# Kernel tuning notes

Hardware: AMD Instinct MI355X
Metric: run time of the kernel (lower is better)

The kernel has to match this reference:

```python
import jax, jax.numpy as jnp
import numpy as np

HEADS = 4
EPS = 1e-5

def _layernorm(x, g, b):
    mu = jnp.mean(x, axis=-1, keepdims=True)
    var = jnp.var(x, axis=-1, keepdims=True)
    return (x - mu) / jnp.sqrt(var + EPS) * g + b

def setup_inputs() -> dict:
    key = jax.random.key(0)
    ks = jax.random.split(key, 16)
    N, dim, k, G = 400000, 256, 1, 4096
    h = jax.random.normal(ks[0], (N, dim), dtype=jnp.float32)
    batch = jnp.sort(jax.random.randint(ks[1], (N,), 0, G).astype(jnp.int64))
    s = 1.0 / np.sqrt(dim)
    return {
        "h": h,
        "batch": batch,
        "num_graphs": G,
        "seed": jax.random.normal(ks[2], (k, dim), dtype=jnp.float32),
        "in_proj_w": jax.random.uniform(ks[3], (3 * dim, dim), minval=-s, maxval=s, dtype=jnp.float32),
        "in_proj_b": jnp.zeros((3 * dim,), jnp.float32),
        "out_w": jax.random.uniform(ks[4], (dim, dim), minval=-s, maxval=s, dtype=jnp.float32),
        "out_b": jnp.zeros((dim,), jnp.float32),
        "w1": jax.random.uniform(ks[5], (4 * dim, dim), minval=-s, maxval=s, dtype=jnp.float32),
        "b1": jnp.zeros((4 * dim,), jnp.float32),
        "w2": jax.random.uniform(ks[6], (dim, 4 * dim), minval=-1.0 / np.sqrt(4 * dim), maxval=1.0 / np.sqrt(4 * dim), dtype=jnp.float32),
        "b2": jnp.zeros((dim,), jnp.float32),
        "g1": jnp.ones((dim,), jnp.float32),
        "beta1": jnp.zeros((dim,), jnp.float32),
        "g2": jnp.ones((dim,), jnp.float32),
        "beta2": jnp.zeros((dim,), jnp.float32),
    }

def reference(h, batch, num_graphs, seed, in_proj_w, in_proj_b, out_w, out_b,
              w1, b1, w2, b2, g1, beta1, g2, beta2):
    N, dim = h.shape
    k = seed.shape[0]
    hd = dim // HEADS
    G = num_graphs
    # q/k/v projections (torch MHA packed in_proj: rows [0:dim]=Q, [dim:2dim]=K, [2dim:]=V)
    q = seed @ in_proj_w[:dim].T + in_proj_b[:dim]                 # [k, dim]
    kk = h @ in_proj_w[dim:2 * dim].T + in_proj_b[dim:2 * dim]     # [N, dim]
    vv = h @ in_proj_w[2 * dim:].T + in_proj_b[2 * dim:]           # [N, dim]
    qh = q.reshape(k, HEADS, hd).transpose(1, 0, 2)                # [H, k, hd]
    kh = kk.reshape(N, HEADS, hd)                                  # [N, H, hd]
    vh = vv.reshape(N, HEADS, hd)                                  # [N, H, hd]
    scale = 1.0 / np.sqrt(hd)
    scores = jnp.einsum('hkd,nhd->nhk', qh, kh) * scale            # [N, H, k]
    # segment softmax over nodes of each graph
    smax = jax.ops.segment_max(scores, batch, num_segments=G)      # [G, H, k]
    e = jnp.exp(scores - smax[batch])                              # [N, H, k]
    denom = jax.ops.segment_sum(e, batch, num_segments=G)          # [G, H, k]
    wv = jax.ops.segment_sum(e[:, :, :, None] * vh[:, :, None, :], batch, num_segments=G)  # [G, H, k, hd]
    attn = jnp.where(denom[..., None] > 0, wv / jnp.maximum(denom, 1e-9)[..., None], 0.0)
    attn = attn.transpose(0, 2, 1, 3).reshape(G, k, dim)           # [G, k, dim]
    o = attn @ out_w.T + out_b                                     # [G, k, dim]
    x = _layernorm(o + seed[None, :, :], g1, beta1)
    f = jax.nn.relu(x @ w1.T + b1) @ w2.T + b2
    x = _layernorm(x + f, g2, beta2)
    # empty graphs output zeros (matches torch loop)
    count = jax.ops.segment_sum(jnp.ones((N,), jnp.float32), batch, num_segments=G)
    return jnp.where((count > 0)[:, None, None], x, 0.0)
```

## Files before the change

### kernel.cpp

```cpp
#include <hip/hip_runtime.h>
#include <hip/hip_bf16.h>


#define DIM 256
#define CHUNK 32

typedef short bf16x8 __attribute__((ext_vector_type(8)));
typedef float f32x4  __attribute__((ext_vector_type(4)));
#define MFMA16(a, b, c) __builtin_amdgcn_mfma_f32_16x16x32_bf16(a, b, c, 0, 0, 0)

#define OFF_C      0
#define OFF_D      1024
#define OFF_CONST  1040
#define OFF_P2B    2048
#define OFF_W1B    133120
#define OFF_W2B    264192
#define OFF_TB     395264
#define OFF_X1     2492416
#define OFF_X1B    3540992
#define OFF_UB     4065280
#define OFF_CNT    6162432

__global__ __launch_bounds__(256) void prep_all_kernel(
    const float* __restrict__ seed, const float* __restrict__ ipw,
    const float* __restrict__ ipb, const float* __restrict__ out_w,
    const float* __restrict__ out_b, const float* __restrict__ w1,
    const float* __restrict__ w2,
    float* __restrict__ cvec, float* __restrict__ dconst,
    float* __restrict__ constvec, __hip_bfloat16* __restrict__ P2b,
    __hip_bfloat16* __restrict__ w1b, __hip_bfloat16* __restrict__ w2b)
{
    int b = blockIdx.x, t = threadIdx.x;
    __shared__ float q_s[DIM];
    if (b < 1024) {
        int i = b >> 2, hD = b & 3;
        float a = 0.f;
        for (int j = 0; j < 64; ++j)
            a += out_w[i * DIM + hD * 64 + j]
               * ipw[(size_t)(2 * DIM + hD * 64 + j) * DIM + t];
        P2b[(size_t)i * 1024 + hD * DIM + t] = __float2bfloat16(a);
    } else if (b == 1024) {
        const float scale = 0.125f;
        float acc = ipb[t];
        for (int d = 0; d < DIM; ++d) acc += seed[d] * ipw[t * DIM + d];
        q_s[t] = acc;
        __syncthreads();
        for (int hh = 0; hh < 4; ++hh) {
            float a = 0.f;
            for (int j = 0; j < 64; ++j)
                a += q_s[hh * 64 + j] * ipw[(size_t)(DIM + hh * 64 + j) * DIM + t];
            cvec[hh * DIM + t] = a * scale;
        }
        if (t < 4) {
            float a = 0.f;
            for (int j = 0; j < 64; ++j)
                a += q_s[t * 64 + j] * ipb[DIM + t * 64 + j];
            dconst[t] = a * scale;
        }
        float cc = out_b[t];
        for (int c = 0; c < DIM; ++c)
            cc += out_w[t * DIM + c] * ipb[2 * DIM + c];
        constvec[t] = cc;
    } else if (b < 1153) {
        int base = (b - 1025) * 2048 + t;
        for (int i = 0; i < 8; ++i)
            w1b[base + i * 256] = __float2bfloat16(w1[base + i * 256]);
    } else {
        int base = (b - 1153) * 2048 + t;
        for (int i = 0; i < 8; ++i)
            w2b[base + i * 256] = __float2bfloat16(w2[base + i * 256]);
    }
}

__global__ __launch_bounds__(256) void attn_pool_kernel(
    const float* __restrict__ hmat, const int* __restrict__ batch,
    const float* __restrict__ cvec, const float* __restrict__ dconst,
    __hip_bfloat16* __restrict__ Tb, int* __restrict__ cnt, int N)
{
    int g = blockIdx.x;
    int tid = threadIdx.x;
    int lane = tid & 63, wave = tid >> 6;

    __shared__ float hbuf[CHUNK][DIM];
    __shared__ float4 esc[CHUNK];
    __shared__ float lred[4][4];

    int s, e;
    { int l = 0, r = N;
      while (l < r) { int m = (l + r) >> 1; if (batch[m] < g) l = m + 1; else r = m; }
      s = l; }
    { int l = s, r = N;
      while (l < r) { int m = (l + r) >> 1; if (batch[m] < g + 1) l = m + 1; else r = m; }
      e = l; }

    if (tid == 0) cnt[g] = e - s;
    size_t tbase = (size_t)g * 1024;
    if (e == s) {
        __hip_bfloat16 z = __float2bfloat16(0.f);
        Tb[tbase + tid] = z; Tb[tbase + 256 + tid] = z;
        Tb[tbase + 512 + tid] = z; Tb[tbase + 768 + tid] = z;
        return;
    }

    int hh = lane & 3, seg = lane >> 2;
    const float* cb = cvec + hh * DIM + seg * 16;
    float4 cr0 = *(const float4*)(cb + 0);
    float4 cr1 = *(const float4*)(cb + 4);
    float4 cr2 = *(const float4*)(cb + 8);
    float4 cr3 = *(const float4*)(cb + 12);
    float dc_mine = dconst[hh];

    float S0 = 0.f, S1 = 0.f, S2 = 0.f, S3 = 0.f;
    float lp = 0.f;

    for (int n0 = s; n0 < e; n0 += CHUNK) {
        int ccnt = min(CHUNK, e - n0);
        for (int idx = tid; idx < ccnt * 64; idx += 256) {
            int j = idx >> 6, q4 = idx & 63;
            float4 v = *(const float4*)&hmat[(size_t)(n0 + j) * DIM + q4 * 4];
            *(float4*)&hbuf[j][q4 * 4] = v;
        }
        __syncthreads();

        for (int j = wave; j < ccnt; j += 4) {
            const float* hb = &hbuf[j][seg * 16];
            float4 h0 = *(const float4*)(hb + 0);
            float4 h1 = *(const float4*)(hb + 4);
            float4 h2 = *(const float4*)(hb + 8);
            float4 h3 = *(const float4*)(hb + 12);
            float p = h0.x * cr0.x + h0.y * cr0.y + h0.z * cr0.z + h0.w * cr0.w
                    + h1.x * cr1.x + h1.y * cr1.y + h1.z * cr1.z + h1.w * cr1.w
                    + h2.x * cr2.x + h2.y * cr2.y + h2.z * cr2.z + h2.w * cr2.w
                    + h3.x * cr3.x + h3.y * cr3.y + h3.z * cr3.z + h3.w * cr3.w;
            p += __shfl_xor(p, 4);
            p += __shfl_xor(p, 8);
            p += __shfl_xor(p, 16);
            p += __shfl_xor(p, 32);
            if (lane < 4) {
                float ev = __expf(p + dc_mine);
                ((float*)&esc[j])[lane] = ev;
                lp += ev;
            }
        }
        __syncthreads();

        for (int j = 0; j < ccnt; ++j) {
            float4 e4 = esc[j];
            float hv = hbuf[j][tid];
            S0 = fmaf(e4.x, hv, S0); S1 = fmaf(e4.y, hv, S1);
            S2 = fmaf(e4.z, hv, S2); S3 = fmaf(e4.w, hv, S3);
        }
        __syncthreads();
    }

    if (lane < 4) lred[wave][lane] = lp;
    __syncthreads();
    float l0 = lred[0][0] + lred[1][0] + lred[2][0] + lred[3][0];
    float l1 = lred[0][1] + lred[1][1] + lred[2][1] + lred[3][1];
    float l2 = lred[0][2] + lred[1][2] + lred[2][2] + lred[3][2];
    float l3 = lred[0][3] + lred[1][3] + lred[2][3] + lred[3][3];
    Tb[tbase + tid]       = __float2bfloat16(S0 / l0);
    Tb[tbase + 256 + tid] = __float2bfloat16(S1 / l1);
    Tb[tbase + 512 + tid] = __float2bfloat16(S2 / l2);
    Tb[tbase + 768 + tid] = __float2bfloat16(S3 / l3);
}

__global__ __launch_bounds__(64) void gemm_o_ln1_kernel(
    const __hip_bfloat16* __restrict__ Tb, const __hip_bfloat16* __restrict__ P2b,
    const float* __restrict__ constvec, const float* __restrict__ seed,
    const float* __restrict__ g1, const float* __restrict__ be1,
    float* __restrict__ x1, __hip_bfloat16* __restrict__ x1b)
{
    int m0 = blockIdx.x * 16;
    int lane = threadIdx.x, quad = lane >> 4, l16 = lane & 15;
    f32x4 acc[16];
#pragma unroll
    for (int i = 0; i < 16; ++i) acc[i] = (f32x4){0.f, 0.f, 0.f, 0.f};
    const __hip_bfloat16* Ap = Tb + (size_t)(m0 + l16) * 1024 + quad * 8;
    const __hip_bfloat16* Bp = P2b + (size_t)l16 * 1024 + quad * 8;
    for (int k0 = 0; k0 < 1024; k0 += 32) {
        bf16x8 a = *(const bf16x8*)(Ap + k0);
#pragma unroll
        for (int nt = 0; nt < 16; ++nt) {
            bf16x8 b = *(const bf16x8*)(Bp + (size_t)nt * 16 * 1024 + k0);
            acc[nt] = MFMA16(a, b, acc[nt]);
        }
    }
    float v[16][4];
    float sum[4] = {0, 0, 0, 0}, sq[4] = {0, 0, 0, 0};
#pragma unroll
    for (int nt = 0; nt < 16; ++nt) {
        int col = nt * 16 + l16;
        float cv = constvec[col] + seed[col];
#pragma unroll
        for (int r = 0; r < 4; ++r) {
            float x = acc[nt][r] + cv;
            v[nt][r] = x; sum[r] += x; sq[r] += x * x;
        }
    }
    float mu_r[4], rs_r[4];
#pragma unroll
    for (int r = 0; r < 4; ++r) {
        float s_ = sum[r], q_ = sq[r];
        s_ += __shfl_xor(s_, 1);  q_ += __shfl_xor(q_, 1);
        s_ += __shfl_xor(s_, 2);  q_ += __shfl_xor(q_, 2);
        s_ += __shfl_xor(s_, 4);  q_ += __shfl_xor(q_, 4);
        s_ += __shfl_xor(s_, 8);  q_ += __shfl_xor(q_, 8);
        float mu = s_ * (1.f / 256);
        float var = q_ * (1.f / 256) - mu * mu;
        mu_r[r] = mu;
        rs_r[r] = rsqrtf(fmaxf(var, 0.f) + 1e-5f);
    }
#pragma unroll
    for (int nt = 0; nt < 16; ++nt) {
        int col = nt * 16 + l16;
        float gg = g1[col], bb = be1[col];
#pragma unroll
        for (int r = 0; r < 4; ++r) {
            int gr = m0 + quad * 4 + r;
            float y = (v[nt][r] - mu_r[r]) * rs_r[r] * gg + bb;
            x1[(size_t)gr * 256 + col] = y;
            x1b[(size_t)gr * 256 + col] = __float2bfloat16(y);
        }
    }
}

__global__ __launch_bounds__(64) void gemm_u_kernel(
    const __hip_bfloat16* __restrict__ x1b, const __hip_bfloat16* __restrict__ w1b,
    const float* __restrict__ b1, __hip_bfloat16* __restrict__ ub)
{
    int m0 = blockIdx.x * 16, nb0 = blockIdx.y * 128;
    int lane = threadIdx.x, quad = lane >> 4, l16 = lane & 15;
    f32x4 acc[8];
#pragma unroll
    for (int i = 0; i < 8; ++i) acc[i] = (f32x4){0.f, 0.f, 0.f, 0.f};
    const __hip_bfloat16* Ap = x1b + (size_t)(m0 + l16) * 256 + quad * 8;
    const __hip_bfloat16* Bp = w1b + (size_t)(nb0 + l16) * 256 + quad * 8;
#pragma unroll
    for (int k0 = 0; k0 < 256; k0 += 32) {
        bf16x8 a = *(const bf16x8*)(Ap + k0);
#pragma unroll
        for (int nt = 0; nt < 8; ++nt) {
            bf16x8 b = *(const bf16x8*)(Bp + (size_t)nt * 16 * 256 + k0);
            acc[nt] = MFMA16(a, b, acc[nt]);
        }
    }
#pragma unroll
    for (int nt = 0; nt < 8; ++nt) {
        int col = nb0 + nt * 16 + l16;
        float bb = b1[col];
#pragma unroll
        for (int r = 0; r < 4; ++r) {
            int gr = m0 + quad * 4 + r;
            float y = fmaxf(acc[nt][r] + bb, 0.f);
            ub[(size_t)gr * 1024 + col] = __float2bfloat16(y);
        }
    }
}

__global__ __launch_bounds__(64) void gemm_f_ln2_kernel(
    const __hip_bfloat16* __restrict__ ub, const __hip_bfloat16* __restrict__ w2b,
    const float* __restrict__ b2, const float* __restrict__ x1,
    const float* __restrict__ g2, const float* __restrict__ be2,
    const int* __restrict__ cnt, float* __restrict__ outp)
{
    int m0 = blockIdx.x * 16;
    int lane = threadIdx.x, quad = lane >> 4, l16 = lane & 15;
    f32x4 acc[16];
#pragma unroll
    for (int i = 0; i < 16; ++i) acc[i] = (f32x4){0.f, 0.f, 0.f, 0.f};
    const __hip_bfloat16* Ap = ub + (size_t)(m0 + l16) * 1024 + quad * 8;
    const __hip_bfloat16* Bp = w2b + (size_t)l16 * 1024 + quad * 8;
    for (int k0 = 0; k0 < 1024; k0 += 32) {
        bf16x8 a = *(const bf16x8*)(Ap + k0);
#pragma unroll
        for (int nt = 0; nt < 16; ++nt) {
            bf16x8 b = *(const bf16x8*)(Bp + (size_t)nt * 16 * 1024 + k0);
            acc[nt] = MFMA16(a, b, acc[nt]);
        }
    }
    float v[16][4];
    float sum[4] = {0, 0, 0, 0}, sq[4] = {0, 0, 0, 0};
#pragma unroll
    for (int nt = 0; nt < 16; ++nt) {
        int col = nt * 16 + l16;
        float bb = b2[col];
#pragma unroll
        for (int r = 0; r < 4; ++r) {
            int gr = m0 + quad * 4 + r;
            float x = acc[nt][r] + bb + x1[(size_t)gr * 256 + col];
            v[nt][r] = x; sum[r] += x; sq[r] += x * x;
        }
    }
    float mu_r[4], rs_r[4];
#pragma unroll
    for (int r = 0; r < 4; ++r) {
        float s_ = sum[r], q_ = sq[r];
        s_ += __shfl_xor(s_, 1);  q_ += __shfl_xor(q_, 1);
        s_ += __shfl_xor(s_, 2);  q_ += __shfl_xor(q_, 2);
        s_ += __shfl_xor(s_, 4);  q_ += __shfl_xor(q_, 4);
        s_ += __shfl_xor(s_, 8);  q_ += __shfl_xor(q_, 8);
        float mu = s_ * (1.f / 256);
        float var = q_ * (1.f / 256) - mu * mu;
        mu_r[r] = mu;
        rs_r[r] = rsqrtf(fmaxf(var, 0.f) + 1e-5f);
    }
#pragma unroll
    for (int r = 0; r < 4; ++r) {
        int gr = m0 + quad * 4 + r;
        float mask = (cnt[gr] > 0) ? 1.f : 0.f;
#pragma unroll
        for (int nt = 0; nt < 16; ++nt) {
            int col = nt * 16 + l16;
            float y = ((v[nt][r] - mu_r[r]) * rs_r[r] * g2[col] + be2[col]) * mask;
            outp[(size_t)gr * 256 + col] = y;
        }
    }
}

extern "C" void kernel_launch(void* const* d_in, const int* in_sizes, int n_in,
                              void* d_out, int out_size, void* d_ws, size_t ws_size,
                              hipStream_t stream) {
    const float* h     = (const float*)d_in[0];
    const int*   batch = (const int*)d_in[1];
    const float* seed  = (const float*)d_in[3];
    const float* ipw   = (const float*)d_in[4];
    const float* ipb   = (const float*)d_in[5];
    const float* out_w = (const float*)d_in[6];
    const float* out_b = (const float*)d_in[7];
    const float* w1    = (const float*)d_in[8];
    const float* b1    = (const float*)d_in[9];
    const float* w2    = (const float*)d_in[10];
    const float* b2    = (const float*)d_in[11];
    const float* g1    = (const float*)d_in[12];
    const float* be1   = (const float*)d_in[13];
    const float* g2    = (const float*)d_in[14];
    const float* be2   = (const float*)d_in[15];

    int N = in_sizes[1];
    int G = out_size / DIM;

    float* ws = (float*)d_ws;
    float* cvec     = ws + OFF_C;
    float* dconst   = ws + OFF_D;
    float* constvec = ws + OFF_CONST;
    __hip_bfloat16* P2b = (__hip_bfloat16*)(ws + OFF_P2B);
    __hip_bfloat16* w1b = (__hip_bfloat16*)(ws + OFF_W1B);
    __hip_bfloat16* w2b = (__hip_bfloat16*)(ws + OFF_W2B);
    __hip_bfloat16* Tb  = (__hip_bfloat16*)(ws + OFF_TB);
    float* x1       = ws + OFF_X1;
    __hip_bfloat16* x1b = (__hip_bfloat16*)(ws + OFF_X1B);
    __hip_bfloat16* ub  = (__hip_bfloat16*)(ws + OFF_UB);
    int*   cnt      = (int*)(ws + OFF_CNT);

    prep_all_kernel<<<1281, 256, 0, stream>>>(seed, ipw, ipb, out_w, out_b, w1, w2,
                                              cvec, dconst, constvec, P2b, w1b, w2b);
    attn_pool_kernel<<<G, 256, 0, stream>>>(h, batch, cvec, dconst, Tb, cnt, N);
    gemm_o_ln1_kernel<<<G / 16, 64, 0, stream>>>(Tb, P2b, constvec, seed, g1, be1,
                                                 x1, x1b);
    gemm_u_kernel<<<dim3(G / 16, 8), 64, 0, stream>>>(x1b, w1b, b1, ub);
    gemm_f_ln2_kernel<<<G / 16, 64, 0, stream>>>(ub, w2b, b2, x1, g2, be2, cnt,
                                                 (float*)d_out);
}
```

Measured before the change: 716.2 us.

## Rewrite attention pooling as single-wave streaming and fuse the three epilogue GEMMs

Segment starts are now computed once in the prep kernel, which removes the per-block binary searches. Attention pooling now runs one 64-thread wave per graph. It streams rows from global memory with register prefetch and keeps all four heads' accumulators in registers, with no LDS staging or block barriers. The out-proj+LN1, FFN up and FFN down+LN2 GEMMs are fused into one kernel, with intermediates held in shared memory, so the global round-trips for x1 and the hidden activations go away. The risks are lower per-graph parallelism in pooling, high register pressure, and the fused epilogue running only G/16 single-wave blocks.

```diff
diff --git a/kernel.cpp b/kernel.cpp
--- a/kernel.cpp
+++ b/kernel.cpp
@@ -3,7 +3,6 @@
 
 
 #define DIM 256
-#define CHUNK 32
 
 typedef short bf16x8 __attribute__((ext_vector_type(8)));
 typedef float f32x4  __attribute__((ext_vector_type(4)));
@@ -16,19 +15,55 @@
 #define OFF_W1B    133120
 #define OFF_W2B    264192
 #define OFF_TB     395264
-#define OFF_X1     2492416
-#define OFF_X1B    3540992
-#define OFF_UB     4065280
-#define OFF_CNT    6162432
+#define OFF_SEG    2492416
+
+__device__ inline float dot16(const float4& a0, const float4& a1,
+                              const float4& a2, const float4& a3,
+                              const float4& b0, const float4& b1,
+                              const float4& b2, const float4& b3) {
+    return a0.x*b0.x + a0.y*b0.y + a0.z*b0.z + a0.w*b0.w
+         + a1.x*b1.x + a1.y*b1.y + a1.z*b1.z + a1.w*b1.w
+         + a2.x*b2.x + a2.y*b2.y + a2.z*b2.z + a2.w*b2.w
+         + a3.x*b3.x + a3.y*b3.y + a3.z*b3.z + a3.w*b3.w;
+}
+
+__device__ inline void fma4(float e, const float4& v, float4& s) {
+    s.x = fmaf(e, v.x, s.x); s.y = fmaf(e, v.y, s.y);
+    s.z = fmaf(e, v.z, s.z); s.w = fmaf(e, v.w, s.w);
+}
+
+__device__ inline float4 xred(float4 a) {
+    a.x += __shfl_xor(a.x, 16); a.y += __shfl_xor(a.y, 16);
+    a.z += __shfl_xor(a.z, 16); a.w += __shfl_xor(a.w, 16);
+    a.x += __shfl_xor(a.x, 32); a.y += __shfl_xor(a.y, 32);
+    a.z += __shfl_xor(a.z, 32); a.w += __shfl_xor(a.w, 32);
+    return a;
+}
+
+__device__ inline float4 sel4(const float4* S, int q) {
+    float4 r = S[0];
+    if (q == 1) r = S[1];
+    if (q == 2) r = S[2];
+    if (q == 3) r = S[3];
+    return r;
+}
+
+__device__ inline unsigned int pk2(float a, float b) {
+    __hip_bfloat16 ha = __float2bfloat16(a), hb = __float2bfloat16(b);
+    unsigned short ua, ub;
+    __builtin_memcpy(&ua, &ha, 2); __builtin_memcpy(&ub, &hb, 2);
+    return (unsigned int)ua | ((unsigned int)ub << 16);
+}
 
 __global__ __launch_bounds__(256) void prep_all_kernel(
     const float* __restrict__ seed, const float* __restrict__ ipw,
     const float* __restrict__ ipb, const float* __restrict__ out_w,
     const float* __restrict__ out_b, const float* __restrict__ w1,
-    const float* __restrict__ w2,
+    const float* __restrict__ w2, const int* __restrict__ batch,
     float* __restrict__ cvec, float* __restrict__ dconst,
     float* __restrict__ constvec, __hip_bfloat16* __restrict__ P2b,
-    __hip_bfloat16* __restrict__ w1b, __hip_bfloat16* __restrict__ w2b)
+    __hip_bfloat16* __restrict__ w1b, __hip_bfloat16* __restrict__ w2b,
+    int* __restrict__ starts, int N, int G)
 {
     int b = blockIdx.x, t = threadIdx.x;
     __shared__ float q_s[DIM];
@@ -65,114 +100,141 @@
         int base = (b - 1025) * 2048 + t;
         for (int i = 0; i < 8; ++i)
             w1b[base + i * 256] = __float2bfloat16(w1[base + i * 256]);
-    } else {
+    } else if (b < 1281) {
         int base = (b - 1153) * 2048 + t;
         for (int i = 0; i < 8; ++i)
             w2b[base + i * 256] = __float2bfloat16(w2[base + i * 256]);
-    }
-}
-
-__global__ __launch_bounds__(256) void attn_pool_kernel(
-    const float* __restrict__ hmat, const int* __restrict__ batch,
+    } else {
+        int i = (b - 1281) * 256 + t;
+        if (i < N) {
+            int bi = batch[i];
+            if (i == 0) {
+                for (int g = 0; g <= bi; ++g) starts[g] = 0;
+            } else {
+                int bp = batch[i - 1];
+                for (int g = bp + 1; g <= bi; ++g) starts[g] = i;
+            }
+            if (i == N - 1)
+                for (int g = bi + 1; g <= G; ++g) starts[g] = N;
+        }
+    }
+}
+
+__global__ __launch_bounds__(64, 2) void attn_pool_kernel(
+    const float* __restrict__ hmat, const int* __restrict__ starts,
     const float* __restrict__ cvec, const float* __restrict__ dconst,
-    __hip_bfloat16* __restrict__ Tb, int* __restrict__ cnt, int N)
+    __hip_bfloat16* __restrict__ Tb)
 {
     int g = blockIdx.x;
-    int tid = threadIdx.x;
-    int lane = tid & 63, wave = tid >> 6;
-
-    __shared__ float hbuf[CHUNK][DIM];
-    __shared__ float4 esc[CHUNK];
-    __shared__ float lred[4][4];
-
-    int s, e;
-    { int l = 0, r = N;
-      while (l < r) { int m = (l + r) >> 1; if (batch[m] < g) l = m + 1; else r = m; }
-      s = l; }
-    { int l = s, r = N;
-      while (l < r) { int m = (l + r) >> 1; if (batch[m] < g + 1) l = m + 1; else r = m; }
-      e = l; }
-
-    if (tid == 0) cnt[g] = e - s;
-    size_t tbase = (size_t)g * 1024;
-    if (e == s) {
-        __hip_bfloat16 z = __float2bfloat16(0.f);
-        Tb[tbase + tid] = z; Tb[tbase + 256 + tid] = z;
-        Tb[tbase + 512 + tid] = z; Tb[tbase + 768 + tid] = z;
-        return;
-    }
-
-    int hh = lane & 3, seg = lane >> 2;
-    const float* cb = cvec + hh * DIM + seg * 16;
-    float4 cr0 = *(const float4*)(cb + 0);
-    float4 cr1 = *(const float4*)(cb + 4);
-    float4 cr2 = *(const float4*)(cb + 8);
-    float4 cr3 = *(const float4*)(cb + 12);
-    float dc_mine = dconst[hh];
-
-    float S0 = 0.f, S1 = 0.f, S2 = 0.f, S3 = 0.f;
-    float lp = 0.f;
-
-    for (int n0 = s; n0 < e; n0 += CHUNK) {
-        int ccnt = min(CHUNK, e - n0);
-        for (int idx = tid; idx < ccnt * 64; idx += 256) {
-            int j = idx >> 6, q4 = idx & 63;
-            float4 v = *(const float4*)&hmat[(size_t)(n0 + j) * DIM + q4 * 4];
-            *(float4*)&hbuf[j][q4 * 4] = v;
-        }
-        __syncthreads();
-
-        for (int j = wave; j < ccnt; j += 4) {
-            const float* hb = &hbuf[j][seg * 16];
-            float4 h0 = *(const float4*)(hb + 0);
-            float4 h1 = *(const float4*)(hb + 4);
-            float4 h2 = *(const float4*)(hb + 8);
-            float4 h3 = *(const float4*)(hb + 12);
-            float p = h0.x * cr0.x + h0.y * cr0.y + h0.z * cr0.z + h0.w * cr0.w
-                    + h1.x * cr1.x + h1.y * cr1.y + h1.z * cr1.z + h1.w * cr1.w
-                    + h2.x * cr2.x + h2.y * cr2.y + h2.z * cr2.z + h2.w * cr2.w
-                    + h3.x * cr3.x + h3.y * cr3.y + h3.z * cr3.z + h3.w * cr3.w;
-            p += __shfl_xor(p, 4);
-            p += __shfl_xor(p, 8);
-            p += __shfl_xor(p, 16);
-            p += __shfl_xor(p, 32);
-            if (lane < 4) {
-                float ev = __expf(p + dc_mine);
-                ((float*)&esc[j])[lane] = ev;
-                lp += ev;
-            }
-        }
-        __syncthreads();
-
-        for (int j = 0; j < ccnt; ++j) {
-            float4 e4 = esc[j];
-            float hv = hbuf[j][tid];
-            S0 = fmaf(e4.x, hv, S0); S1 = fmaf(e4.y, hv, S1);
-            S2 = fmaf(e4.z, hv, S2); S3 = fmaf(e4.w, hv, S3);
-        }
-        __syncthreads();
-    }
-
-    if (lane < 4) lred[wave][lane] = lp;
-    __syncthreads();
-    float l0 = lred[0][0] + lred[1][0] + lred[2][0] + lred[3][0];
-    float l1 = lred[0][1] + lred[1][1] + lred[2][1] + lred[3][1];
-    float l2 = lred[0][2] + lred[1][2] + lred[2][2] + lred[3][2];
-    float l3 = lred[0][3] + lred[1][3] + lred[2][3] + lred[3][3];
-    Tb[tbase + tid]       = __float2bfloat16(S0 / l0);
-    Tb[tbase + 256 + tid] = __float2bfloat16(S1 / l1);
-    Tb[tbase + 512 + tid] = __float2bfloat16(S2 / l2);
-    Tb[tbase + 768 + tid] = __float2bfloat16(S3 / l3);
-}
-
-__global__ __launch_bounds__(64) void gemm_o_ln1_kernel(
+    int lane = threadIdx.x;
+    int gq = lane >> 4, l16 = lane & 15;
+
+    int s = starts[g], e = starts[g + 1];
+
+    float4 c0[4], c1[4], c2[4], c3[4];
+    const float* cb = cvec + l16 * 16;
+#pragma unroll
+    for (int hh = 0; hh < 4; ++hh) {
+        c0[hh] = *(const float4*)(cb + hh * DIM + 0);
+        c1[hh] = *(const float4*)(cb + hh * DIM + 4);
+        c2[hh] = *(const float4*)(cb + hh * DIM + 8);
+        c3[hh] = *(const float4*)(cb + hh * DIM + 12);
+    }
+    float dc0 = dconst[0], dc1 = dconst[1], dc2 = dconst[2], dc3 = dconst[3];
+
+    float4 S0[4], S1[4], S2[4], S3[4];
+#pragma unroll
+    for (int hh = 0; hh < 4; ++hh) {
+        S0[hh] = make_float4(0, 0, 0, 0); S1[hh] = make_float4(0, 0, 0, 0);
+        S2[hh] = make_float4(0, 0, 0, 0); S3[hh] = make_float4(0, 0, 0, 0);
+    }
+    float l0 = 0.f, l1 = 0.f, l2 = 0.f, l3 = 0.f;
+
+    if (e > s) {
+        int nc = min(s + gq, e - 1);
+        const float* hp = hmat + (size_t)nc * DIM + l16 * 16;
+        float4 v0 = *(const float4*)(hp + 0);
+        float4 v1 = *(const float4*)(hp + 4);
+        float4 v2 = *(const float4*)(hp + 8);
+        float4 v3 = *(const float4*)(hp + 12);
+        for (int nb = s; nb < e; nb += 4) {
+            bool valid = (nb + gq) < e;
+            int nn = min(nb + 4 + gq, e - 1);
+            const float* hq = hmat + (size_t)nn * DIM + l16 * 16;
+            float4 w0 = *(const float4*)(hq + 0);
+            float4 w1v = *(const float4*)(hq + 4);
+            float4 w2v = *(const float4*)(hq + 8);
+            float4 w3 = *(const float4*)(hq + 12);
+
+            float p0 = dot16(v0, v1, v2, v3, c0[0], c1[0], c2[0], c3[0]);
+            float p1 = dot16(v0, v1, v2, v3, c0[1], c1[1], c2[1], c3[1]);
+            float p2 = dot16(v0, v1, v2, v3, c0[2], c1[2], c2[2], c3[2]);
+            float p3 = dot16(v0, v1, v2, v3, c0[3], c1[3], c2[3], c3[3]);
+            p0 += __shfl_xor(p0, 1); p0 += __shfl_xor(p0, 2);
+            p0 += __shfl_xor(p0, 4); p0 += __shfl_xor(p0, 8);
+            p1 += __shfl_xor(p1, 1); p1 += __shfl_xor(p1, 2);
+            p1 += __shfl_xor(p1, 4); p1 += __shfl_xor(p1, 8);
+            p2 += __shfl_xor(p2, 1); p2 += __shfl_xor(p2, 2);
+            p2 += __shfl_xor(p2, 4); p2 += __shfl_xor(p2, 8);
+            p3 += __shfl_xor(p3, 1); p3 += __shfl_xor(p3, 2);
+            p3 += __shfl_xor(p3, 4); p3 += __shfl_xor(p3, 8);
+
+            float e0 = valid ? __expf(p0 + dc0) : 0.f;
+            float e1 = valid ? __expf(p1 + dc1) : 0.f;
+            float e2 = valid ? __expf(p2 + dc2) : 0.f;
+            float e3 = valid ? __expf(p3 + dc3) : 0.f;
+            l0 += e0; l1 += e1; l2 += e2; l3 += e3;
+
+            fma4(e0, v0, S0[0]); fma4(e0, v1, S1[0]);
+            fma4(e0, v2, S2[0]); fma4(e0, v3, S3[0]);
+            fma4(e1, v0, S0[1]); fma4(e1, v1, S1[1]);
+            fma4(e1, v2, S2[1]); fma4(e1, v3, S3[1]);
+            fma4(e2, v0, S0[2]); fma4(e2, v1, S1[2]);
+            fma4(e2, v2, S2[2]); fma4(e2, v3, S3[2]);
+            fma4(e3, v0, S0[3]); fma4(e3, v1, S1[3]);
+            fma4(e3, v2, S2[3]); fma4(e3, v3, S3[3]);
+
+            v0 = w0; v1 = w1v; v2 = w2v; v3 = w3;
+        }
+    }
+
+#pragma unroll
+    for (int hh = 0; hh < 4; ++hh) {
+        S0[hh] = xred(S0[hh]); S1[hh] = xred(S1[hh]);
+        S2[hh] = xred(S2[hh]); S3[hh] = xred(S3[hh]);
+    }
+    l0 += __shfl_xor(l0, 16); l0 += __shfl_xor(l0, 32);
+    l1 += __shfl_xor(l1, 16); l1 += __shfl_xor(l1, 32);
+    l2 += __shfl_xor(l2, 16); l2 += __shfl_xor(l2, 32);
+    l3 += __shfl_xor(l3, 16); l3 += __shfl_xor(l3, 32);
+
+    float lv = gq == 0 ? l0 : gq == 1 ? l1 : gq == 2 ? l2 : l3;
+    float iv = (lv > 0.f) ? 1.f / lv : 0.f;
+    float4 A0 = sel4(S0, gq), A1 = sel4(S1, gq);
+    float4 A2 = sel4(S2, gq), A3 = sel4(S3, gq);
+    uint4 o0, o1;
+    o0.x = pk2(A0.x * iv, A0.y * iv); o0.y = pk2(A0.z * iv, A0.w * iv);
+    o0.z = pk2(A1.x * iv, A1.y * iv); o0.w = pk2(A1.z * iv, A1.w * iv);
+    o1.x = pk2(A2.x * iv, A2.y * iv); o1.y = pk2(A2.z * iv, A2.w * iv);
+    o1.z = pk2(A3.x * iv, A3.y * iv); o1.w = pk2(A3.z * iv, A3.w * iv);
+    uint4* tp = (uint4*)(Tb + (size_t)g * 1024 + gq * 256 + l16 * 16);
+    tp[0] = o0; tp[1] = o1;
+}
+
+__global__ __launch_bounds__(64) void epilogue_kernel(
     const __hip_bfloat16* __restrict__ Tb, const __hip_bfloat16* __restrict__ P2b,
+    const __hip_bfloat16* __restrict__ w1b, const __hip_bfloat16* __restrict__ w2b,
     const float* __restrict__ constvec, const float* __restrict__ seed,
     const float* __restrict__ g1, const float* __restrict__ be1,
-    float* __restrict__ x1, __hip_bfloat16* __restrict__ x1b)
+    const float* __restrict__ b1, const float* __restrict__ b2,
+    const float* __restrict__ g2, const float* __restrict__ be2,
+    const int* __restrict__ starts, float* __restrict__ outp)
 {
     int m0 = blockIdx.x * 16;
     int lane = threadIdx.x, quad = lane >> 4, l16 = lane & 15;
+    __shared__ __hip_bfloat16 x1s[16][264];
+    __shared__ __hip_bfloat16 us[16][1048];
+
     f32x4 acc[16];
 #pragma unroll
     for (int i = 0; i < 16; ++i) acc[i] = (f32x4){0.f, 0.f, 0.f, 0.f};
@@ -208,8 +270,7 @@
         s_ += __shfl_xor(s_, 8);  q_ += __shfl_xor(q_, 8);
         float mu = s_ * (1.f / 256);
         float var = q_ * (1.f / 256) - mu * mu;
-        mu_r[r] = mu;
-        rs_r[r] = rsqrtf(fmaxf(var, 0.f) + 1e-5f);
+        mu_r[r] = mu; rs_r[r] = rsqrtf(fmaxf(var, 0.f) + 1e-5f);
     }
 #pragma unroll
     for (int nt = 0; nt < 16; ++nt) {
@@ -217,98 +278,76 @@
         float gg = g1[col], bb = be1[col];
 #pragma unroll
         for (int r = 0; r < 4; ++r) {
-            int gr = m0 + quad * 4 + r;
             float y = (v[nt][r] - mu_r[r]) * rs_r[r] * gg + bb;
-            x1[(size_t)gr * 256 + col] = y;
-            x1b[(size_t)gr * 256 + col] = __float2bfloat16(y);
-        }
-    }
-}
-
-__global__ __launch_bounds__(64) void gemm_u_kernel(
-    const __hip_bfloat16* __restrict__ x1b, const __hip_bfloat16* __restrict__ w1b,
-    const float* __restrict__ b1, __hip_bfloat16* __restrict__ ub)
-{
-    int m0 = blockIdx.x * 16, nb0 = blockIdx.y * 128;
-    int lane = threadIdx.x, quad = lane >> 4, l16 = lane & 15;
-    f32x4 acc[8];
-#pragma unroll
-    for (int i = 0; i < 8; ++i) acc[i] = (f32x4){0.f, 0.f, 0.f, 0.f};
-    const __hip_bfloat16* Ap = x1b + (size_t)(m0 + l16) * 256 + quad * 8;
-    const __hip_bfloat16* Bp = w1b + (size_t)(nb0 + l16) * 256 + quad * 8;
-#pragma unroll
-    for (int k0 = 0; k0 < 256; k0 += 32) {
-        bf16x8 a = *(const bf16x8*)(Ap + k0);
-#pragma unroll
-        for (int nt = 0; nt < 8; ++nt) {
-            bf16x8 b = *(const bf16x8*)(Bp + (size_t)nt * 16 * 256 + k0);
-            acc[nt] = MFMA16(a, b, acc[nt]);
-        }
-    }
-#pragma unroll
-    for (int nt = 0; nt < 8; ++nt) {
-        int col = nb0 + nt * 16 + l16;
-        float bb = b1[col];
-#pragma unroll
-        for (int r = 0; r < 4; ++r) {
-            int gr = m0 + quad * 4 + r;
-            float y = fmaxf(acc[nt][r] + bb, 0.f);
-            ub[(size_t)gr * 1024 + col] = __float2bfloat16(y);
-        }
-    }
-}
-
-__global__ __launch_bounds__(64) void gemm_f_ln2_kernel(
-    const __hip_bfloat16* __restrict__ ub, const __hip_bfloat16* __restrict__ w2b,
-    const float* __restrict__ b2, const float* __restrict__ x1,
-    const float* __restrict__ g2, const float* __restrict__ be2,
-    const int* __restrict__ cnt, float* __restrict__ outp)
-{
-    int m0 = blockIdx.x * 16;
-    int lane = threadIdx.x, quad = lane >> 4, l16 = lane & 15;
-    f32x4 acc[16];
-#pragma unroll
-    for (int i = 0; i < 16; ++i) acc[i] = (f32x4){0.f, 0.f, 0.f, 0.f};
-    const __hip_bfloat16* Ap = ub + (size_t)(m0 + l16) * 1024 + quad * 8;
-    const __hip_bfloat16* Bp = w2b + (size_t)l16 * 1024 + quad * 8;
+            v[nt][r] = y;
+            x1s[quad * 4 + r][col] = __float2bfloat16(y);
+        }
+    }
+    __syncthreads();
+
+    for (int c4 = 0; c4 < 4; ++c4) {
+        f32x4 ua[16];
+#pragma unroll
+        for (int i = 0; i < 16; ++i) ua[i] = (f32x4){0.f, 0.f, 0.f, 0.f};
+        const __hip_bfloat16* Bp1 = w1b + (size_t)(c4 * 256 + l16) * 256 + quad * 8;
+#pragma unroll
+        for (int k0 = 0; k0 < 256; k0 += 32) {
+            bf16x8 a = *(const bf16x8*)&x1s[l16][k0 + quad * 8];
+#pragma unroll
+            for (int nt = 0; nt < 16; ++nt) {
+                bf16x8 b = *(const bf16x8*)(Bp1 + (size_t)nt * 16 * 256 + k0);
+                ua[nt] = MFMA16(a, b, ua[nt]);
+            }
+        }
+#pragma unroll
+        for (int nt = 0; nt < 16; ++nt) {
+            int col = c4 * 256 + nt * 16 + l16;
+            float bb = b1[col];
+#pragma unroll
+            for (int r = 0; r < 4; ++r)
+                us[quad * 4 + r][col] = __float2bfloat16(fmaxf(ua[nt][r] + bb, 0.f));
+        }
+    }
+    __syncthreads();
+
+    f32x4 fa[16];
+#pragma unroll
+    for (int i = 0; i < 16; ++i) fa[i] = (f32x4){0.f, 0.f, 0.f, 0.f};
+    const __hip_bfloat16* Bp2 = w2b + (size_t)l16 * 1024 + quad * 8;
     for (int k0 = 0; k0 < 1024; k0 += 32) {
-        bf16x8 a = *(const bf16x8*)(Ap + k0);
+        bf16x8 a = *(const bf16x8*)&us[l16][k0 + quad * 8];
 #pragma unroll
         for (int nt = 0; nt < 16; ++nt) {
-            bf16x8 b = *(const bf16x8*)(Bp + (size_t)nt * 16 * 1024 + k0);
-            acc[nt] = MFMA16(a, b, acc[nt]);
-        }
-    }
-    float v[16][4];
-    float sum[4] = {0, 0, 0, 0}, sq[4] = {0, 0, 0, 0};
+            bf16x8 b = *(const bf16x8*)(Bp2 + (size_t)nt * 16 * 1024 + k0);
+            fa[nt] = MFMA16(a, b, fa[nt]);
+        }
+    }
+    float sum2[4] = {0, 0, 0, 0}, sq2[4] = {0, 0, 0, 0};
 #pragma unroll
     for (int nt = 0; nt < 16; ++nt) {
         int col = nt * 16 + l16;
         float bb = b2[col];
 #pragma unroll
         for (int r = 0; r < 4; ++r) {
-            int gr = m0 + quad * 4 + r;
-            float x = acc[nt][r] + bb + x1[(size_t)gr * 256 + col];
-            v[nt][r] = x; sum[r] += x; sq[r] += x * x;
-        }
-    }
-    float mu_r[4], rs_r[4];
+            float x = fa[nt][r] + bb + v[nt][r];
+            v[nt][r] = x; sum2[r] += x; sq2[r] += x * x;
+        }
+    }
 #pragma unroll
     for (int r = 0; r < 4; ++r) {
-        float s_ = sum[r], q_ = sq[r];
+        float s_ = sum2[r], q_ = sq2[r];
         s_ += __shfl_xor(s_, 1);  q_ += __shfl_xor(q_, 1);
         s_ += __shfl_xor(s_, 2);  q_ += __shfl_xor(q_, 2);
         s_ += __shfl_xor(s_, 4);  q_ += __shfl_xor(q_, 4);
         s_ += __shfl_xor(s_, 8);  q_ += __shfl_xor(q_, 8);
         float mu = s_ * (1.f / 256);
         float var = q_ * (1.f / 256) - mu * mu;
-        mu_r[r] = mu;
-        rs_r[r] = rsqrtf(fmaxf(var, 0.f) + 1e-5f);
+        mu_r[r] = mu; rs_r[r] = rsqrtf(fmaxf(var, 0.f) + 1e-5f);
     }
 #pragma unroll
     for (int r = 0; r < 4; ++r) {
         int gr = m0 + quad * 4 + r;
-        float mask = (cnt[gr] > 0) ? 1.f : 0.f;
+        float mask = (starts[gr + 1] > starts[gr]) ? 1.f : 0.f;
 #pragma unroll
         for (int nt = 0; nt < 16; ++nt) {
             int col = nt * 16 + l16;
@@ -348,17 +387,14 @@
     __hip_bfloat16* w1b = (__hip_bfloat16*)(ws + OFF_W1B);
     __hip_bfloat16* w2b = (__hip_bfloat16*)(ws + OFF_W2B);
     __hip_bfloat16* Tb  = (__hip_bfloat16*)(ws + OFF_TB);
-    float* x1       = ws + OFF_X1;
-    __hip_bfloat16* x1b = (__hip_bfloat16*)(ws + OFF_X1B);
-    __hip_bfloat16* ub  = (__hip_bfloat16*)(ws + OFF_UB);
-    int*   cnt      = (int*)(ws + OFF_CNT);
-
-    prep_all_kernel<<<1281, 256, 0, stream>>>(seed, ipw, ipb, out_w, out_b, w1, w2,
-                                              cvec, dconst, constvec, P2b, w1b, w2b);
-    attn_pool_kernel<<<G, 256, 0, stream>>>(h, batch, cvec, dconst, Tb, cnt, N);
-    gemm_o_ln1_kernel<<<G / 16, 64, 0, stream>>>(Tb, P2b, constvec, seed, g1, be1,
-                                                 x1, x1b);
-    gemm_u_kernel<<<dim3(G / 16, 8), 64, 0, stream>>>(x1b, w1b, b1, ub);
-    gemm_f_ln2_kernel<<<G / 16, 64, 0, stream>>>(ub, w2b, b2, x1, g2, be2, cnt,
-                                                 (float*)d_out);
-}
+    int* starts     = (int*)(ws + OFF_SEG);
+
+    int seg_blocks = (N + 255) / 256;
+    prep_all_kernel<<<1281 + seg_blocks, 256, 0, stream>>>(
+        seed, ipw, ipb, out_w, out_b, w1, w2, batch,
+        cvec, dconst, constvec, P2b, w1b, w2b, starts, N, G);
+    attn_pool_kernel<<<G, 64, 0, stream>>>(h, starts, cvec, dconst, Tb);
+    epilogue_kernel<<<G / 16, 64, 0, stream>>>(Tb, P2b, w1b, w2b, constvec, seed,
+                                               g1, be1, b1, b2, g2, be2, starts,
+                                               (float*)d_out);
+}
```

Result: slower. 779.6 us (+8.8%).
